# Kernel optimization log

Measured on AMD Instinct MI355X. Metric: run time of the kernel, lower is better.

## Reference

```python
import jax, jax.numpy as jnp
import numpy as np

N_NODES = 20000
D = 512
H = 8
DK = D // H  # 64
L = 2


def _layernorm(x, g, b, eps=1e-5):
    mu = x.mean(-1, keepdims=True)
    var = x.var(-1, keepdims=True)
    return (x - mu) / jnp.sqrt(var + eps) * g + b


def _hgt_layer(h, kw, kb, qw, qb, vw, vb, aw, ab, pri, att_r, msg_r, skip, ln_g, ln_b, src, dst):
    # h: [N, D]
    N = h.shape[0]
    k = (h @ kw.T + kb).reshape(N, H, DK)
    q = (h @ qw.T + qb).reshape(N, H, DK)
    v = (h @ vw.T + vb).reshape(N, H, DK)
    # per-relation bilinear transforms on keys and messages
    k = jnp.einsum('nhi,hij->nhj', k, att_r)
    v = jnp.einsum('nhi,hij->nhj', v, msg_r)
    # per-edge attention scores [E, H]
    t = jnp.einsum('ehd,ehd->eh', k[src], q[dst]) * pri / jnp.sqrt(jnp.float32(DK))
    # edge softmax over incoming edges of each destination node
    mx = jax.ops.segment_max(t, dst, num_segments=N)
    e = jnp.exp(t - mx[dst])
    den = jax.ops.segment_sum(e, dst, num_segments=N)
    att = e / jnp.maximum(den[dst], 1e-9)
    # weighted message aggregation [N, H, DK] -> [N, D]
    msg = v[src] * att[..., None]
    agg = jax.ops.segment_sum(msg, dst, num_segments=N).reshape(N, D)
    trans = jax.nn.gelu(agg) @ aw.T + ab
    alpha = jax.nn.sigmoid(skip)
    out = trans * alpha + h * (1.0 - alpha)
    return _layernorm(out, ln_g, ln_b)


def setup_inputs() -> dict:
    key = jax.random.key(0)
    ks = jax.random.split(key, 16)
    B, E = 8192, 320000
    s = 0.02
    inp = {
        'embeddings': jax.random.normal(ks[0], (B, D), jnp.float32),
        'node_emb': jax.random.normal(ks[1], (N_NODES, D), jnp.float32) * s,
        'adapt_w': jax.random.normal(ks[2], (D, D), jnp.float32) * s,
        'adapt_b': jnp.zeros((D,), jnp.float32),
        'kw': jax.random.normal(ks[3], (L, D, D), jnp.float32) * s,
        'kb': jnp.zeros((L, D), jnp.float32),
        'qw': jax.random.normal(ks[4], (L, D, D), jnp.float32) * s,
        'qb': jnp.zeros((L, D), jnp.float32),
        'vw': jax.random.normal(ks[5], (L, D, D), jnp.float32) * s,
        'vb': jnp.zeros((L, D), jnp.float32),
        'aw': jax.random.normal(ks[6], (L, D, D), jnp.float32) * s,
        'ab': jnp.zeros((L, D), jnp.float32),
        'pri': jnp.ones((L, H), jnp.float32),
        'att_r': jax.random.normal(ks[7], (L, H, DK, DK), jnp.float32) * (1.0 / np.sqrt(DK)),
        'msg_r': jax.random.normal(ks[8], (L, H, DK, DK), jnp.float32) * (1.0 / np.sqrt(DK)),
        'skip': jnp.ones((L,), jnp.float32),
        'ln_g': jnp.ones((L, D), jnp.float32),
        'ln_b': jnp.zeros((L, D), jnp.float32),
        'out_w': jax.random.normal(ks[9], (D, D), jnp.float32) * s,
        'out_b': jnp.zeros((D,), jnp.float32),
        'attn_kernels': jax.random.uniform(ks[10], (D,), jnp.float32),
        'src': jax.random.randint(ks[11], (E,), 0, N_NODES, jnp.int32),
        'dst': jax.random.randint(ks[12], (E,), 0, N_NODES, jnp.int32),
        'n_classes': 10000,
    }
    return inp


def reference(embeddings, node_emb, adapt_w, adapt_b, kw, kb, qw, qb, vw, vb, aw, ab,
              pri, att_r, msg_r, skip, ln_g, ln_b, out_w, out_b, attn_kernels,
              src, dst, n_classes):
    # Hgt encoder over the label graph (single ntype '_N')
    h = jax.nn.gelu(node_emb @ adapt_w.T + adapt_b)
    for l in range(L):
        h = _hgt_layer(h, kw[l], kb[l], qw[l], qb[l], vw[l], vb[l], aw[l], ab[l],
                       pri[l], att_r[l], msg_r[l], skip[l], ln_g[l], ln_b[l], src, dst)
    cls_emb = h @ out_w.T + out_b          # [N, D]
    cls_emb = cls_emb[:n_classes]          # [C, D]  (dropout is identity in eval)
    # logits[b,c] = sum_d embeddings[b,d] * attn_kernels[d] * cls_emb[c,d]
    logits = (embeddings * attn_kernels) @ cls_emb.T
    return logits
```

## Files before the change

kernel.cpp:

```cpp
#include <hip/hip_runtime.h>
#include <hip/hip_bf16.h>

#define D 512
#define H 8
#define NLAYER 2

typedef __attribute__((ext_vector_type(8))) short short8;
typedef __attribute__((ext_vector_type(4))) short short4v;
typedef __attribute__((ext_vector_type(4))) float f32x4;

__device__ __forceinline__ float gelu_f(float x) {
    float x3 = x * x * x;
    return 0.5f * x * (1.0f + tanhf(0.7978845608028654f * (x + 0.044715f * x3)));
}

__device__ __forceinline__ unsigned short f2b(float x) {
    unsigned u = __float_as_uint(x);
    u += 0x7FFF + ((u >> 16) & 1);
    return (unsigned short)(u >> 16);
}
__device__ __forceinline__ float b2f(unsigned short u) {
    return __uint_as_float(((unsigned)u) << 16);
}

template <int POSTG, int OUTMODE>
__global__ __launch_bounds__(256) void gemm_bf(
    const short* __restrict__ A, const short* __restrict__ B,
    const float* __restrict__ bias, float* __restrict__ Cf,
    short* __restrict__ Cb, int M, int N, int K) {
    __shared__ __align__(16) short As[128 * 72];
    __shared__ __align__(16) short Bs[128 * 72];
    const unsigned gx = gridDim.x, gy = gridDim.y;
    const unsigned nwg = gx * gy;
    const unsigned orig = blockIdx.y * gx + blockIdx.x;
    const unsigned q = nwg >> 3, r = nwg & 7;
    const unsigned xcd = orig & 7, sidx = orig >> 3;
    const unsigned swz = (xcd < r ? xcd * (q + 1) : r * (q + 1) + (xcd - r) * q) + sidx;
    const unsigned CH = 8;
    const unsigned chunk = swz / (CH * gx);
    const unsigned rem = swz - chunk * (CH * gx);
    const unsigned nr = min(CH, gy - chunk * CH);
    const unsigned col = rem / nr;
    const unsigned rowin = rem - col * nr;
    const int bm = (int)(chunk * CH + rowin) * 128;
    const int bn = (int)col * 128;

    const int tid = threadIdx.x;
    const int lane = tid & 63;
    const int wave = tid >> 6;
    const int wm = (wave >> 1) * 64, wn = (wave & 1) * 64;
    const int lr16 = lane & 15;
    const int lk8 = (lane >> 4) * 8;

    const int srow = tid >> 1;
    const int skb = (tid & 1) * 32;
    const int arow = min(bm + srow, M - 1);
    const int brow = min(bn + srow, N - 1);
    const short* Ap = A + (size_t)arow * K + skb;
    const short* Bp = B + (size_t)brow * K + skb;

    f32x4 acc[4][4];
#pragma unroll
    for (int i = 0; i < 4; ++i)
#pragma unroll
        for (int j = 0; j < 4; ++j) acc[i][j] = (f32x4){0.f, 0.f, 0.f, 0.f};

    short8 ra[4], rb[4];
    auto load_ab = [&](int k0) {
#pragma unroll
        for (int u = 0; u < 4; ++u) {
            ra[u] = *(const short8*)(Ap + k0 + u * 8);
            rb[u] = *(const short8*)(Bp + k0 + u * 8);
        }
    };

    load_ab(0);
    for (int k0 = 0; k0 < K; k0 += 64) {
        __syncthreads();
#pragma unroll
        for (int u = 0; u < 4; ++u) {
            *(short8*)&As[srow * 72 + skb + u * 8] = ra[u];
            *(short8*)&Bs[srow * 72 + skb + u * 8] = rb[u];
        }
        __syncthreads();
        if (k0 + 64 < K) load_ab(k0 + 64);

#pragma unroll
        for (int kk = 0; kk < 2; ++kk) {
            short8 af[4], bfr[4];
#pragma unroll
            for (int mi = 0; mi < 4; ++mi)
                af[mi] = *(const short8*)&As[(wm + mi * 16 + lr16) * 72 + kk * 32 + lk8];
#pragma unroll
            for (int ni = 0; ni < 4; ++ni)
                bfr[ni] = *(const short8*)&Bs[(wn + ni * 16 + lr16) * 72 + kk * 32 + lk8];
#pragma unroll
            for (int mi = 0; mi < 4; ++mi)
#pragma unroll
                for (int ni = 0; ni < 4; ++ni)
                    acc[mi][ni] = __builtin_amdgcn_mfma_f32_16x16x32_bf16(
                        af[mi], bfr[ni], acc[mi][ni], 0, 0, 0);
        }
    }

#pragma unroll
    for (int mi = 0; mi < 4; ++mi) {
        int row0 = bm + wm + mi * 16 + (lane >> 4) * 4;
#pragma unroll
        for (int ni = 0; ni < 4; ++ni) {
            int col2 = bn + wn + ni * 16 + lr16;
            if (col2 < N) {
                float bsv = bias ? bias[col2] : 0.0f;
#pragma unroll
                for (int rr2 = 0; rr2 < 4; ++rr2) {
                    int row = row0 + rr2;
                    if (row < M) {
                        float v = acc[mi][ni][rr2] + bsv;
                        if (POSTG) v = gelu_f(v);
                        if (OUTMODE != 1) Cf[(size_t)row * N + col2] = v;
                        if (OUTMODE != 0) Cb[(size_t)row * N + col2] = (short)f2b(v);
                    }
                }
            }
        }
    }
}

__global__ void cvt_b16(const float* __restrict__ in, short* __restrict__ out, int n8) {
    int i = blockIdx.x * 256 + threadIdx.x;
    if (i >= n8) return;
    float4 a = ((const float4*)in)[i * 2];
    float4 b = ((const float4*)in)[i * 2 + 1];
    short8 o;
    o[0] = f2b(a.x); o[1] = f2b(a.y); o[2] = f2b(a.z); o[3] = f2b(a.w);
    o[4] = f2b(b.x); o[5] = f2b(b.y); o[6] = f2b(b.z); o[7] = f2b(b.w);
    *(short8*)(out + (size_t)i * 8) = o;
}

__global__ void cp_f32(const float* __restrict__ in, float* __restrict__ out, int n) {
    int i = blockIdx.x * 256 + threadIdx.x;
    if (i < n) out[i] = in[i];
}

__global__ __launch_bounds__(256) void fuse_w(
    const float* __restrict__ w, const float* __restrict__ bsrc,
    const float* __restrict__ r, short* __restrict__ fw, float* __restrict__ fb) {
    int h = blockIdx.y;
    int dc = blockIdx.x * 64;
    __shared__ float rs[64][64];
    int tid = threadIdx.x;
    for (int i = tid; i < 4096; i += 256) rs[i >> 6][i & 63] = r[h * 4096 + i];
    __syncthreads();
    for (int rep = 0; rep < 16; ++rep) {
        int o = rep * 256 + tid;
        int j = o >> 6;
        int dd = o & 63;
        float s = 0.0f;
#pragma unroll 8
        for (int i = 0; i < 64; ++i)
            s = fmaf(rs[i][j], w[(size_t)(h * 64 + i) * D + dc + dd], s);
        fw[(size_t)(h * 64 + j) * D + dc + dd] = (short)f2b(s);
    }
    if (blockIdx.x == 0 && tid < 64) {
        float s = 0.0f;
        for (int i = 0; i < 64; ++i) s += bsrc[h * 64 + i] * rs[i][tid];
        fb[h * 64 + tid] = s;
    }
}

__global__ void zero_int(int* __restrict__ p, int n) {
    int i = blockIdx.x * 256 + threadIdx.x;
    if (i < n) p[i] = 0;
}

__global__ void hist_dst(const int* __restrict__ dst, int* __restrict__ cnt, int E) {
    int i = blockIdx.x * 256 + threadIdx.x;
    if (i < E) atomicAdd(&cnt[dst[i]], 1);
}

__global__ __launch_bounds__(1024) void scan_counts(
    const int* __restrict__ cnt, int* __restrict__ offs, int* __restrict__ cursor,
    int n, int E) {
    __shared__ int part[1024];
    int t = threadIdx.x;
    int chunk = (n + 1023) >> 10;
    int lo = t * chunk;
    int hi = min(lo + chunk, n);
    int s = 0;
    for (int i = lo; i < hi; ++i) s += cnt[i];
    part[t] = s;
    __syncthreads();
    for (int off = 1; off < 1024; off <<= 1) {
        int v = (t >= off) ? part[t - off] : 0;
        __syncthreads();
        part[t] += v;
        __syncthreads();
    }
    int base = (t == 0) ? 0 : part[t - 1];
    for (int i = lo; i < hi; ++i) {
        offs[i] = base;
        cursor[i] = base;
        base += cnt[i];
    }
    if (t == 1023) offs[n] = E;
}

__global__ void scatter_edges(const int* __restrict__ src, const int* __restrict__ dst,
                              int* __restrict__ cursor, int* __restrict__ srcs, int E) {
    int i = blockIdx.x * 256 + threadIdx.x;
    if (i < E) {
        int pos = atomicAdd(&cursor[dst[i]], 1);
        srcs[pos] = src[i];
    }
}

__global__ __launch_bounds__(256) void edge_attn(
    const short* __restrict__ kqv, const int* __restrict__ srcs,
    const int* __restrict__ offs, const float* __restrict__ pri,
    short* __restrict__ gg, int NNodes) {
    int n = blockIdx.x * 4 + (threadIdx.x >> 6);
    if (n >= NNodes) return;
    int lane = threadIdx.x & 63;
    int start = offs[n], end = offs[n + 1];

    const short8 qv = *(const short8*)(kqv + (size_t)n * 1536 + 512 + lane * 8);
    float qf[8];
#pragma unroll
    for (int j = 0; j < 8; ++j) qf[j] = b2f((unsigned short)qv[j]);
    const float prih = pri[lane >> 3] * 0.125f;

    float rm = -INFINITY, rden = 0.0f;
    float vacc[8];
#pragma unroll
    for (int j = 0; j < 8; ++j) vacc[j] = 0.0f;

    for (int i = start; i < end; ++i) {
        int sn = srcs[i];
        const short* row = kqv + (size_t)sn * 1536;
        short8 kv = *(const short8*)(row + lane * 8);
        short8 vv = *(const short8*)(row + 1024 + lane * 8);
        float sum = 0.0f;
#pragma unroll
        for (int j = 0; j < 8; ++j)
            sum = fmaf(b2f((unsigned short)kv[j]), qf[j], sum);
        sum += __shfl_xor(sum, 1);
        sum += __shfl_xor(sum, 2);
        sum += __shfl_xor(sum, 4);
        float tt = sum * prih;
        float nm = fmaxf(rm, tt);
        float scl = expf(rm - nm);
        float e = expf(tt - nm);
        rden = rden * scl + e;
        rm = nm;
#pragma unroll
        for (int j = 0; j < 8; ++j)
            vacc[j] = fmaf(vacc[j], scl, b2f((unsigned short)vv[j]) * e);
    }

    float inv = 1.0f / fmaxf(rden, 1e-9f);
    unsigned o[4];
#pragma unroll
    for (int p = 0; p < 4; ++p) {
        float s0 = gelu_f(vacc[2 * p] * inv);
        float s1 = gelu_f(vacc[2 * p + 1] * inv);
        o[p] = (unsigned)(unsigned short)f2b(s0) |
               ((unsigned)(unsigned short)f2b(s1) << 16);
    }
    uint4 pack = make_uint4(o[0], o[1], o[2], o[3]);
    *(uint4*)(gg + (size_t)n * D + lane * 8) = pack;
}

__global__ __launch_bounds__(128) void blend_ln(
    const float* __restrict__ trans, const float* __restrict__ hin,
    const float* __restrict__ skip, const float* __restrict__ g,
    const float* __restrict__ b, float* __restrict__ hout,
    short* __restrict__ hb16) {
    int n = blockIdx.x;
    int tid = threadIdx.x;
    float alpha = 1.0f / (1.0f + expf(-skip[0]));
    size_t base = (size_t)n * D + tid * 4;
    float4 t4 = *(const float4*)(trans + base);
    float4 h4 = *(const float4*)(hin + base);
    float o[4];
    o[0] = t4.x * alpha + h4.x * (1.0f - alpha);
    o[1] = t4.y * alpha + h4.y * (1.0f - alpha);
    o[2] = t4.z * alpha + h4.z * (1.0f - alpha);
    o[3] = t4.w * alpha + h4.w * (1.0f - alpha);
    float s = o[0] + o[1] + o[2] + o[3];
    float ss = o[0] * o[0] + o[1] * o[1] + o[2] * o[2] + o[3] * o[3];
    for (int off = 32; off; off >>= 1) {
        s += __shfl_down(s, off);
        ss += __shfl_down(ss, off);
    }
    __shared__ float red[4];
    if ((tid & 63) == 0) { red[tid >> 6] = s; red[2 + (tid >> 6)] = ss; }
    __syncthreads();
    float S = red[0] + red[1];
    float SS = red[2] + red[3];
    float mu = S * (1.0f / 512.0f);
    float var = SS * (1.0f / 512.0f) - mu * mu;
    float inv = rsqrtf(var + 1e-5f);
    int c = tid * 4;
    float4 o4;
    o4.x = (o[0] - mu) * inv * g[c + 0] + b[c + 0];
    o4.y = (o[1] - mu) * inv * g[c + 1] + b[c + 1];
    o4.z = (o[2] - mu) * inv * g[c + 2] + b[c + 2];
    o4.w = (o[3] - mu) * inv * g[c + 3] + b[c + 3];
    *(float4*)(hout + base) = o4;
    short4v hb;
    hb[0] = f2b(o4.x); hb[1] = f2b(o4.y); hb[2] = f2b(o4.z); hb[3] = f2b(o4.w);
    *(short4v*)(hb16 + base) = hb;
}

__global__ void scale_emb_b16(const float* __restrict__ e, const float* __restrict__ ak,
                              short* __restrict__ o, int n8) {
    int i = blockIdx.x * 256 + threadIdx.x;
    if (i >= n8) return;
    float4 a = ((const float4*)e)[i * 2];
    float4 b = ((const float4*)e)[i * 2 + 1];
    int d0 = (i * 8) & (D - 1);
    short8 v;
    v[0] = f2b(a.x * ak[d0 + 0]); v[1] = f2b(a.y * ak[d0 + 1]);
    v[2] = f2b(a.z * ak[d0 + 2]); v[3] = f2b(a.w * ak[d0 + 3]);
    v[4] = f2b(b.x * ak[d0 + 4]); v[5] = f2b(b.y * ak[d0 + 5]);
    v[6] = f2b(b.z * ak[d0 + 6]); v[7] = f2b(b.w * ak[d0 + 7]);
    *(short8*)(o + (size_t)i * 8) = v;
}

extern "C" void kernel_launch(void* const* d_in, const int* in_sizes, int n_in,
                              void* d_out, int out_size, void* d_ws, size_t ws_size,
                              hipStream_t stream) {
    const float* embeddings = (const float*)d_in[0];
    const float* node_emb   = (const float*)d_in[1];
    const float* adapt_w    = (const float*)d_in[2];
    const float* adapt_b    = (const float*)d_in[3];
    const float* kw   = (const float*)d_in[4];
    const float* kb   = (const float*)d_in[5];
    const float* qw   = (const float*)d_in[6];
    const float* qb   = (const float*)d_in[7];
    const float* vw   = (const float*)d_in[8];
    const float* vb   = (const float*)d_in[9];
    const float* aw   = (const float*)d_in[10];
    const float* ab   = (const float*)d_in[11];
    const float* pri  = (const float*)d_in[12];
    const float* att_r = (const float*)d_in[13];
    const float* msg_r = (const float*)d_in[14];
    const float* skip  = (const float*)d_in[15];
    const float* ln_g  = (const float*)d_in[16];
    const float* ln_b  = (const float*)d_in[17];
    const float* out_w = (const float*)d_in[18];
    const float* out_b = (const float*)d_in[19];
    const float* attn_k = (const float*)d_in[20];
    const int* src = (const int*)d_in[21];
    const int* dst = (const int*)d_in[22];

    const int E  = in_sizes[21];
    const int NB = in_sizes[0] / D;
    const int NN = in_sizes[1] / D;
    const int NC = out_size / NB;

    size_t big = (size_t)NN * D;
    float* hbuf = (float*)d_ws;
    float* fb32 = hbuf + big;
    short* hb16 = (short*)(fb32 + big);
    short* gg16 = hb16 + big;
    short* kqv16 = gg16 + big;
    short* w16a = kqv16 + (size_t)NN * 1536;
    short* w16o = w16a + (size_t)D * D;
    short* w16w = w16o + (size_t)D * D;
    short* wcat = w16w + (size_t)D * D;
    float* bcat = (float*)(wcat + (size_t)1536 * D);
    int* offs   = (int*)(bcat + 1536);
    int* cursor = offs + NN + 1;
    int* srcs   = cursor + NN;
    short* cls16 = kqv16;
    short* embs16 = kqv16 + (size_t)NC * D;

    auto ggrid = [](int M, int N) { return dim3((N + 127) / 128, (M + 127) / 128); };
    const int WB = D * D / 8;

    zero_int<<<(NN + 255) / 256, 256, 0, stream>>>(cursor, NN);
    hist_dst<<<(E + 255) / 256, 256, 0, stream>>>(dst, cursor, E);
    scan_counts<<<1, 1024, 0, stream>>>(cursor, offs, cursor, NN, E);
    scatter_edges<<<(E + 255) / 256, 256, 0, stream>>>(src, dst, cursor, srcs, E);

    cvt_b16<<<((int)(big / 8) + 255) / 256, 256, 0, stream>>>(node_emb, gg16, (int)(big / 8));
    cvt_b16<<<(WB + 255) / 256, 256, 0, stream>>>(adapt_w, w16a, WB);
    cvt_b16<<<(WB + 255) / 256, 256, 0, stream>>>(out_w, w16o, WB);

    gemm_bf<1, 2><<<ggrid(NN, D), 256, 0, stream>>>(gg16, w16a, adapt_b, hbuf, hb16, NN, D, D);

    for (int l = 0; l < NLAYER; ++l) {
        const size_t wo = (size_t)l * D * D;
        fuse_w<<<dim3(8, 8), 256, 0, stream>>>(kw + wo, kb + l * D, att_r + (size_t)l * H * 64 * 64, wcat, bcat);
        cvt_b16<<<(WB + 255) / 256, 256, 0, stream>>>(qw + wo, wcat + (size_t)512 * D, WB);
        cp_f32<<<2, 256, 0, stream>>>(qb + l * D, bcat + 512, D);
        fuse_w<<<dim3(8, 8), 256, 0, stream>>>(vw + wo, vb + l * D, msg_r + (size_t)l * H * 64 * 64, wcat + (size_t)1024 * D, bcat + 1024);

        gemm_bf<0, 1><<<ggrid(NN, 1536), 256, 0, stream>>>(hb16, wcat, bcat, nullptr, kqv16, NN, 1536, D);

        edge_attn<<<(NN + 3) / 4, 256, 0, stream>>>(kqv16, srcs, offs, pri + l * H, gg16, NN);

        cvt_b16<<<(WB + 255) / 256, 256, 0, stream>>>(aw + wo, w16w, WB);
        gemm_bf<0, 0><<<ggrid(NN, D), 256, 0, stream>>>(gg16, w16w, ab + l * D, fb32, nullptr, NN, D, D);
        blend_ln<<<NN, 128, 0, stream>>>(fb32, hbuf, skip + l, ln_g + l * D, ln_b + l * D, hbuf, hb16);
    }

    gemm_bf<0, 1><<<ggrid(NC, D), 256, 0, stream>>>(hb16, w16o, out_b, nullptr, cls16, NC, D, D);
    scale_emb_b16<<<((NB * D / 8) + 255) / 256, 256, 0, stream>>>(embeddings, attn_k, embs16, NB * D / 8);
    gemm_bf<0, 0><<<ggrid(NB, NC), 256, 0, stream>>>(embs16, cls16, nullptr, (float*)d_out, nullptr, NB, NC, D);
}
```

Baseline: 875.1 us.

## Stream GEMM tiles with direct global-to-LDS loads and dual-edge softmax

```diff
diff --git a/kernel.cpp b/kernel.cpp
--- a/kernel.cpp
+++ b/kernel.cpp
@@ -21,6 +21,12 @@
 }
 __device__ __forceinline__ float b2f(unsigned short u) {
     return __uint_as_float(((unsigned)u) << 16);
+}
+
+__device__ __forceinline__ void gld16(const short* g, short* l) {
+    __builtin_amdgcn_global_load_lds(
+        (const __attribute__((address_space(1))) void*)g,
+        (__attribute__((address_space(3))) void*)l, 16, 0, 0);
 }
 
 template <int POSTG, int OUTMODE>
@@ -28,8 +34,8 @@
     const short* __restrict__ A, const short* __restrict__ B,
     const float* __restrict__ bias, float* __restrict__ Cf,
     short* __restrict__ Cb, int M, int N, int K) {
-    __shared__ __align__(16) short As[128 * 72];
-    __shared__ __align__(16) short Bs[128 * 72];
+    __shared__ __align__(16) short As[2][4096];
+    __shared__ __align__(16) short Bs[2][4096];
     const unsigned gx = gridDim.x, gy = gridDim.y;
     const unsigned nwg = gx * gy;
     const unsigned orig = blockIdx.y * gx + blockIdx.x;
@@ -52,12 +58,19 @@
     const int lr16 = lane & 15;
     const int lk8 = (lane >> 4) * 8;
 
-    const int srow = tid >> 1;
-    const int skb = (tid & 1) * 32;
-    const int arow = min(bm + srow, M - 1);
-    const int brow = min(bn + srow, N - 1);
-    const short* Ap = A + (size_t)arow * K + skb;
-    const short* Bp = B + (size_t)brow * K + skb;
+    const int trow = tid >> 2;
+    const int tchk = (tid & 3) * 8;
+    const short* a0 = A + (size_t)min(bm + trow, M - 1) * K + tchk;
+    const short* a1 = A + (size_t)min(bm + 64 + trow, M - 1) * K + tchk;
+    const short* b0 = B + (size_t)min(bn + trow, N - 1) * K + tchk;
+    const short* b1 = B + (size_t)min(bn + 64 + trow, N - 1) * K + tchk;
+
+    auto stage = [&](int buf, int k0) {
+        gld16(a0 + k0, &As[buf][tid * 8]);
+        gld16(a1 + k0, &As[buf][2048 + tid * 8]);
+        gld16(b0 + k0, &Bs[buf][tid * 8]);
+        gld16(b1 + k0, &Bs[buf][2048 + tid * 8]);
+    };
 
     f32x4 acc[4][4];
 #pragma unroll
@@ -65,42 +78,26 @@
 #pragma unroll
         for (int j = 0; j < 4; ++j) acc[i][j] = (f32x4){0.f, 0.f, 0.f, 0.f};
 
-    short8 ra[4], rb[4];
-    auto load_ab = [&](int k0) {
-#pragma unroll
-        for (int u = 0; u < 4; ++u) {
-            ra[u] = *(const short8*)(Ap + k0 + u * 8);
-            rb[u] = *(const short8*)(Bp + k0 + u * 8);
-        }
-    };
-
-    load_ab(0);
-    for (int k0 = 0; k0 < K; k0 += 64) {
+    stage(0, 0);
+    int cur = 0;
+    for (int k0 = 0; k0 < K; k0 += 32) {
         __syncthreads();
-#pragma unroll
-        for (int u = 0; u < 4; ++u) {
-            *(short8*)&As[srow * 72 + skb + u * 8] = ra[u];
-            *(short8*)&Bs[srow * 72 + skb + u * 8] = rb[u];
-        }
-        __syncthreads();
-        if (k0 + 64 < K) load_ab(k0 + 64);
-
-#pragma unroll
-        for (int kk = 0; kk < 2; ++kk) {
-            short8 af[4], bfr[4];
-#pragma unroll
-            for (int mi = 0; mi < 4; ++mi)
-                af[mi] = *(const short8*)&As[(wm + mi * 16 + lr16) * 72 + kk * 32 + lk8];
+        if (k0 + 32 < K) stage(cur ^ 1, k0 + 32);
+
+        short8 af[4], bfr[4];
+#pragma unroll
+        for (int mi = 0; mi < 4; ++mi)
+            af[mi] = *(const short8*)&As[cur][(wm + mi * 16 + lr16) * 32 + lk8];
+#pragma unroll
+        for (int ni = 0; ni < 4; ++ni)
+            bfr[ni] = *(const short8*)&Bs[cur][(wn + ni * 16 + lr16) * 32 + lk8];
+#pragma unroll
+        for (int mi = 0; mi < 4; ++mi)
 #pragma unroll
             for (int ni = 0; ni < 4; ++ni)
-                bfr[ni] = *(const short8*)&Bs[(wn + ni * 16 + lr16) * 72 + kk * 32 + lk8];
-#pragma unroll
-            for (int mi = 0; mi < 4; ++mi)
-#pragma unroll
-                for (int ni = 0; ni < 4; ++ni)
-                    acc[mi][ni] = __builtin_amdgcn_mfma_f32_16x16x32_bf16(
-                        af[mi], bfr[ni], acc[mi][ni], 0, 0, 0);
-        }
+                acc[mi][ni] = __builtin_amdgcn_mfma_f32_16x16x32_bf16(
+                    af[mi], bfr[ni], acc[mi][ni], 0, 0, 0);
+        cur ^= 1;
     }
 
 #pragma unroll
@@ -229,42 +226,73 @@
     for (int j = 0; j < 8; ++j) qf[j] = b2f((unsigned short)qv[j]);
     const float prih = pri[lane >> 3] * 0.125f;
 
-    float rm = -INFINITY, rden = 0.0f;
-    float vacc[8];
-#pragma unroll
-    for (int j = 0; j < 8; ++j) vacc[j] = 0.0f;
-
-    for (int i = start; i < end; ++i) {
-        int sn = srcs[i];
-        const short* row = kqv + (size_t)sn * 1536;
-        short8 kv = *(const short8*)(row + lane * 8);
-        short8 vv = *(const short8*)(row + 1024 + lane * 8);
-        float sum = 0.0f;
+    float rm0 = -INFINITY, rd0 = 0.0f, rm1 = -INFINITY, rd1 = 0.0f;
+    float va0[8], va1[8];
+#pragma unroll
+    for (int j = 0; j < 8; ++j) { va0[j] = 0.0f; va1[j] = 0.0f; }
+
+    int i = start;
+    for (; i + 1 < end; i += 2) {
+        int s0 = srcs[i], s1 = srcs[i + 1];
+        const short* r0 = kqv + (size_t)s0 * 1536;
+        const short* r1 = kqv + (size_t)s1 * 1536;
+        short8 k0 = *(const short8*)(r0 + lane * 8);
+        short8 v0 = *(const short8*)(r0 + 1024 + lane * 8);
+        short8 k1 = *(const short8*)(r1 + lane * 8);
+        short8 v1 = *(const short8*)(r1 + 1024 + lane * 8);
+        float d0 = 0.0f, d1 = 0.0f;
+#pragma unroll
+        for (int j = 0; j < 8; ++j) {
+            d0 = fmaf(b2f((unsigned short)k0[j]), qf[j], d0);
+            d1 = fmaf(b2f((unsigned short)k1[j]), qf[j], d1);
+        }
+        d0 += __shfl_xor(d0, 1); d1 += __shfl_xor(d1, 1);
+        d0 += __shfl_xor(d0, 2); d1 += __shfl_xor(d1, 2);
+        d0 += __shfl_xor(d0, 4); d1 += __shfl_xor(d1, 4);
+        float t0 = d0 * prih, t1 = d1 * prih;
+        float nm0 = fmaxf(rm0, t0), nm1 = fmaxf(rm1, t1);
+        float sc0 = expf(rm0 - nm0), sc1 = expf(rm1 - nm1);
+        float e0 = expf(t0 - nm0), e1 = expf(t1 - nm1);
+        rd0 = rd0 * sc0 + e0; rm0 = nm0;
+        rd1 = rd1 * sc1 + e1; rm1 = nm1;
+#pragma unroll
+        for (int j = 0; j < 8; ++j) {
+            va0[j] = fmaf(va0[j], sc0, b2f((unsigned short)v0[j]) * e0);
+            va1[j] = fmaf(va1[j], sc1, b2f((unsigned short)v1[j]) * e1);
+        }
+    }
+    if (i < end) {
+        int s0 = srcs[i];
+        const short* r0 = kqv + (size_t)s0 * 1536;
+        short8 k0 = *(const short8*)(r0 + lane * 8);
+        short8 v0 = *(const short8*)(r0 + 1024 + lane * 8);
+        float d0 = 0.0f;
+#pragma unroll
+        for (int j = 0; j < 8; ++j) d0 = fmaf(b2f((unsigned short)k0[j]), qf[j], d0);
+        d0 += __shfl_xor(d0, 1);
+        d0 += __shfl_xor(d0, 2);
+        d0 += __shfl_xor(d0, 4);
+        float t0 = d0 * prih;
+        float nm0 = fmaxf(rm0, t0);
+        float sc0 = expf(rm0 - nm0);
+        float e0 = expf(t0 - nm0);
+        rd0 = rd0 * sc0 + e0; rm0 = nm0;
 #pragma unroll
         for (int j = 0; j < 8; ++j)
-            sum = fmaf(b2f((unsigned short)kv[j]), qf[j], sum);
-        sum += __shfl_xor(sum, 1);
-        sum += __shfl_xor(sum, 2);
-        sum += __shfl_xor(sum, 4);
-        float tt = sum * prih;
-        float nm = fmaxf(rm, tt);
-        float scl = expf(rm - nm);
-        float e = expf(tt - nm);
-        rden = rden * scl + e;
-        rm = nm;
-#pragma unroll
-        for (int j = 0; j < 8; ++j)
-            vacc[j] = fmaf(vacc[j], scl, b2f((unsigned short)vv[j]) * e);
-    }
-
+            va0[j] = fmaf(va0[j], sc0, b2f((unsigned short)v0[j]) * e0);
+    }
+
+    float m = fmaxf(fmaxf(rm0, rm1), -3.0e38f);
+    float s0 = expf(rm0 - m), s1 = expf(rm1 - m);
+    float rden = rd0 * s0 + rd1 * s1;
     float inv = 1.0f / fmaxf(rden, 1e-9f);
     unsigned o[4];
 #pragma unroll
     for (int p = 0; p < 4; ++p) {
-        float s0 = gelu_f(vacc[2 * p] * inv);
-        float s1 = gelu_f(vacc[2 * p + 1] * inv);
-        o[p] = (unsigned)(unsigned short)f2b(s0) |
-               ((unsigned)(unsigned short)f2b(s1) << 16);
+        float x0 = gelu_f((va0[2 * p] * s0 + va1[2 * p] * s1) * inv);
+        float x1 = gelu_f((va0[2 * p + 1] * s0 + va1[2 * p + 1] * s1) * inv);
+        o[p] = (unsigned)(unsigned short)f2b(x0) |
+               ((unsigned)(unsigned short)f2b(x1) << 16);
     }
     uint4 pack = make_uint4(o[0], o[1], o[2], o[3]);
     *(uint4*)(gg + (size_t)n * D + lane * 8) = pack;
```

Result: no change. 861.8 us (-1.5%).
